# Kernel tuning notes

Hardware: AMD Instinct MI355X
Metric: run time of the kernel (lower is better)

## Reference

```python
import jax, jax.numpy as jnp
import numpy as np

NUM_EXPERTS = 8
TOP_K = 2


def setup_inputs() -> dict:
    key = jax.random.key(0)
    k0, k1, k2, k3, k4 = jax.random.split(key, 5)
    T, D, F, E = 4096, 2048, 4096, NUM_EXPERTS  # tokens, hidden, intermediate, experts
    s_in = 1.0 / np.sqrt(D).astype(np.float32)
    s_mid = 1.0 / np.sqrt(F).astype(np.float32)
    return {
        "hidden_states": jax.random.normal(k0, (T, D), jnp.float32),
        "gate_w": jax.random.normal(k1, (D, E), jnp.float32) * s_in,   # router gate (no bias)
        "w1": jax.random.normal(k2, (E, D, F), jnp.float32) * s_in,     # expert gate proj
        "w3": jax.random.normal(k3, (E, D, F), jnp.float32) * s_in,     # expert up proj
        "w2": jax.random.normal(k4, (E, F, D), jnp.float32) * s_mid,    # expert down proj
    }


def reference(hidden_states, gate_w, w1, w3, w2):
    x = hidden_states  # [T, D] (original flattens any leading dims)
    # Router: logits in fp32 (router_logits.float()), softmax over ALL experts,
    # take top-k WITHOUT renormalization (renormalize=False).
    logits = (x @ gate_w).astype(jnp.float32)            # [T, E]
    probs = jax.nn.softmax(logits, axis=-1)              # [T, E]
    topk_w, topk_i = jax.lax.top_k(probs, TOP_K)         # [T, K]
    # Dense combine weights: zero for non-selected experts. [T, E]
    combine = jnp.sum(
        jax.nn.one_hot(topk_i, NUM_EXPERTS, dtype=x.dtype) * topk_w[..., None],
        axis=1,
    )

    # SwiGLU experts, vmapped over the expert axis (fixed, small E).
    def expert_fn(w1e, w3e, w2e):
        return (jax.nn.silu(x @ w1e) * (x @ w3e)) @ w2e  # [T, D]

    expert_out = jax.vmap(expert_fn)(w1, w3, w2)         # [E, T, D]
    return jnp.einsum("te,etd->td", combine, expert_out)  # [T, D]
```

## Files before the change

kernel.cpp:

```cpp
#include <hip/hip_runtime.h>
#include <hip/hip_bf16.h>

#define TK 4096
#define DD 2048
#define FF 4096
#define NE 8
#define BM 128
#define BN 128
#define BKR 32
#define BKP 64

typedef __attribute__((ext_vector_type(8))) short bf16x8;
typedef __attribute__((ext_vector_type(4))) short bf16x4;
typedef __attribute__((ext_vector_type(4))) float f32x4;

__device__ __forceinline__ unsigned short f2bf(float f) {
  return __builtin_bit_cast(unsigned short, __float2bfloat16(f));
}
__device__ __forceinline__ float bf2f(unsigned short u) {
  return __builtin_bit_cast(float, (unsigned)u << 16);
}

__device__ __forceinline__ void gl16(const unsigned short* g, unsigned short* l) {
  __builtin_amdgcn_global_load_lds(
      (const __attribute__((address_space(1))) unsigned int*)g,
      (__attribute__((address_space(3))) unsigned int*)l, 16, 0, 0);
}

#define VMCNT(n) asm volatile("s_waitcnt vmcnt(" #n ")" ::: "memory")
#define SBAR()   __builtin_amdgcn_s_barrier()

__device__ __forceinline__ int g_swz(int row) { return ((row >> 1) & 3) ^ ((row >> 3) & 3); }
__device__ __forceinline__ int swzoff(int row, int bir) {
  return row * 64 + ((((bir >> 4) ^ g_swz(row)) & 3) << 4) + (bir & 15);
}
__device__ __forceinline__ int permB(int f) {
  return (f & 0x60) | ((f & 3) << 3) | ((f >> 2) & 7);
}

__global__ void k_router(const float* __restrict__ x, const float* __restrict__ gw,
                         int* __restrict__ cnt, int* __restrict__ ltok,
                         float* __restrict__ lw, unsigned short* __restrict__ xb,
                         int2* __restrict__ t2s) {
  int tok = (blockIdx.x * blockDim.x + threadIdx.x) >> 6;
  int lane = threadIdx.x & 63;
  if (tok >= TK) return;
  const float* xr = x + (size_t)tok * DD;
  float a0=0,a1=0,a2=0,a3=0,a4=0,a5=0,a6=0,a7=0;
  for (int p = 0; p < DD / 256; ++p) {
    int d0 = p * 256 + lane * 4;
    f32x4 xv = *(const f32x4*)(xr + d0);
    if (xb) {
      bf16x4 t;
      t[0] = (short)f2bf(xv[0]); t[1] = (short)f2bf(xv[1]);
      t[2] = (short)f2bf(xv[2]); t[3] = (short)f2bf(xv[3]);
      *(bf16x4*)(xb + (size_t)tok * DD + d0) = t;
    }
#pragma unroll
    for (int j = 0; j < 4; ++j) {
      float xs = xv[j];
      const f32x4* g = (const f32x4*)(gw + (size_t)(d0 + j) * NE);
      f32x4 g0 = g[0], g1 = g[1];
      a0 += xs * g0[0]; a1 += xs * g0[1]; a2 += xs * g0[2]; a3 += xs * g0[3];
      a4 += xs * g1[0]; a5 += xs * g1[1]; a6 += xs * g1[2]; a7 += xs * g1[3];
    }
  }
#pragma unroll
  for (int s = 32; s > 0; s >>= 1) {
    a0 += __shfl_xor(a0, s, 64); a1 += __shfl_xor(a1, s, 64);
    a2 += __shfl_xor(a2, s, 64); a3 += __shfl_xor(a3, s, 64);
    a4 += __shfl_xor(a4, s, 64); a5 += __shfl_xor(a5, s, 64);
    a6 += __shfl_xor(a6, s, 64); a7 += __shfl_xor(a7, s, 64);
  }
  if (lane == 0) {
    float p_[NE] = {a0, a1, a2, a3, a4, a5, a6, a7};
    float m = p_[0];
#pragma unroll
    for (int e = 1; e < NE; ++e) m = fmaxf(m, p_[e]);
    float ssum = 0.f;
#pragma unroll
    for (int e = 0; e < NE; ++e) { p_[e] = __expf(p_[e] - m); ssum += p_[e]; }
    float inv = 1.f / ssum;
    int i1 = 0; float b1 = p_[0];
#pragma unroll
    for (int e = 1; e < NE; ++e) if (p_[e] > b1) { b1 = p_[e]; i1 = e; }
    int i2 = -1; float b2 = -1.f;
#pragma unroll
    for (int e = 0; e < NE; ++e) if (e != i1 && p_[e] > b2) { b2 = p_[e]; i2 = e; }
    int s1 = atomicAdd(&cnt[i1], 1);
    ltok[i1 * TK + s1] = tok; lw[i1 * TK + s1] = b1 * inv;
    int s2 = atomicAdd(&cnt[i2], 1);
    ltok[i2 * TK + s2] = tok; lw[i2 * TK + s2] = b2 * inv;
    if (t2s) t2s[tok] = make_int2(i1 * TK + s1, i2 * TK + s2);
  }
}

__global__ void k_prefix(const int* __restrict__ cnt, int* __restrict__ off) {
  if (threadIdx.x == 0) {
    int a = 0;
#pragma unroll
    for (int e = 0; e < NE; ++e) { off[e] = a; a += cnt[e]; }
    off[NE] = a;
  }
}

__global__ __launch_bounds__(256)
void k_tr(const float* __restrict__ src0, unsigned short* __restrict__ dst0,
          int R, int C) {
  const int e = blockIdx.z;
  const float* src = src0 + (size_t)e * R * C;
  unsigned short* dst = dst0 + (size_t)e * R * C;
  const int tid = threadIdx.x;
  const int w = tid >> 6, lane = tid & 63;
  const int r0 = blockIdx.y * 256 + w * 64 + (lane >> 3) * 8;
  const int c0 = blockIdx.x * 32 + (lane & 7) * 4;
  f32x4 v[8];
#pragma unroll
  for (int j = 0; j < 8; ++j) v[j] = *(const f32x4*)(src + (size_t)(r0 + j) * C + c0);
#pragma unroll
  for (int jc = 0; jc < 4; ++jc) {
    bf16x8 o;
#pragma unroll
    for (int j = 0; j < 8; ++j) o[j] = (short)f2bf(v[j][jc]);
    *(bf16x8*)(dst + (size_t)(c0 + jc) * R + r0) = o;
  }
}

__global__ __launch_bounds__(256)
void k_tr13(const float* __restrict__ w1, const float* __restrict__ w3,
            unsigned short* __restrict__ d1, unsigned short* __restrict__ d3) {
  const int z = blockIdx.z;
  const int e = z & (NE - 1);
  const float* src = (z < NE ? w1 : w3) + (size_t)e * DD * FF;
  unsigned short* dst = (z < NE ? d1 : d3) + (size_t)e * DD * FF;
  const int tid = threadIdx.x;
  const int w = tid >> 6, lane = tid & 63;
  const int r0 = blockIdx.y * 256 + w * 64 + (lane >> 3) * 8;
  const int c0 = blockIdx.x * 32 + (lane & 7) * 4;
  f32x4 v[8];
#pragma unroll
  for (int j = 0; j < 8; ++j) v[j] = *(const f32x4*)(src + (size_t)(r0 + j) * FF + c0);
#pragma unroll
  for (int jc = 0; jc < 4; ++jc) {
    bf16x8 o;
#pragma unroll
    for (int j = 0; j < 8; ++j) o[j] = (short)f2bf(v[j][jc]);
    *(bf16x8*)(dst + (size_t)(c0 + jc) * DD + r0) = o;
  }
}

__global__ __launch_bounds__(256)
void k_comb(const unsigned short* __restrict__ O, const int2* __restrict__ t2s,
            const int* __restrict__ off, float* __restrict__ out) {
  const int idx = blockIdx.x * 256 + threadIdx.x;
  const int t = idx >> 8;
  const int d0 = (idx & 255) * 8;
  const int2 v = t2s[t];
  const int s1 = off[v.x >> 12] + (v.x & (TK - 1));
  const int s2 = off[v.y >> 12] + (v.y & (TK - 1));
  bf16x8 a = *(const bf16x8*)(O + (size_t)s1 * DD + d0);
  bf16x8 b = *(const bf16x8*)(O + (size_t)s2 * DD + d0);
  f32x4 r0, r1;
#pragma unroll
  for (int j = 0; j < 4; ++j) {
    r0[j] = bf2f((unsigned short)a[j]) + bf2f((unsigned short)b[j]);
    r1[j] = bf2f((unsigned short)a[j + 4]) + bf2f((unsigned short)b[j + 4]);
  }
  float* o = out + (size_t)t * DD + d0;
  *(f32x4*)o = r0;
  *(f32x4*)(o + 4) = r1;
}


__global__ __launch_bounds__(256, 2)
void k_gemm1g(const unsigned short* __restrict__ xb, const unsigned short* __restrict__ w1t,
              const unsigned short* __restrict__ w3t, const int* __restrict__ cnt,
              const int* __restrict__ off, const int* __restrict__ ltok,
              const float* __restrict__ lw, unsigned short* __restrict__ H) {
  const int e = blockIdx.z;
  const int ce = cnt[e];
  const int m0 = blockIdx.y * BM;
  if (m0 >= ce) return;
  const int n0 = blockIdx.x * BN;
  const int tid = threadIdx.x, lane = tid & 63, w = tid >> 6;
  const int wr = w >> 1, wc = w & 1;
  const unsigned short* W1 = w1t + (size_t)e * FF * DD;
  const unsigned short* W3 = w3t + (size_t)e * FF * DD;
  const int base = off[e];

  __shared__ __align__(16) unsigned short As[BM * BKP];
  __shared__ __align__(16) unsigned short B1s[2][BM * BKP];
  __shared__ __align__(16) unsigned short B3s[2][BM * BKP];

  const int swz8 = ((lane & 7) ^ ((lane >> 3) & 7)) * 8;
  const unsigned short *aSrc[4], *b1Src[4], *b3Src[4];
#pragma unroll
  for (int i = 0; i < 4; ++i) {
    int row = w * 32 + i * 8 + (lane >> 3);
    int gm = m0 + row;
    int tok = (gm < ce) ? ltok[e * TK + gm] : ltok[e * TK];
    aSrc[i]  = xb + (size_t)tok * DD + swz8;
    b1Src[i] = W1 + (size_t)(n0 + row) * DD + swz8;
    b3Src[i] = W3 + (size_t)(n0 + row) * DD + swz8;
  }

  const int kc = lane >> 4;
  int aOff[4][2], bOff[4][2];
#pragma unroll
  for (int m = 0; m < 4; ++m) {
    int row = wr * 64 + m * 16 + (lane & 15);
#pragma unroll
    for (int kk = 0; kk < 2; ++kk) {
      int c = kk * 4 + kc;
      aOff[m][kk] = row * 128 + ((c ^ (row & 7)) << 4);
    }
  }
#pragma unroll
  for (int n = 0; n < 4; ++n) {
    int row = wc * 64 + n * 16 + (lane & 15);
#pragma unroll
    for (int kk = 0; kk < 2; ++kk) {
      int c = kk * 4 + kc;
      bOff[n][kk] = row * 128 + ((c ^ (row & 7)) << 4);
    }
  }

  f32x4 acc1[4][4], acc3[4][4];
#pragma unroll
  for (int m = 0; m < 4; ++m)
#pragma unroll
    for (int n = 0; n < 4; ++n)
#pragma unroll
      for (int j = 0; j < 4; ++j) { acc1[m][n][j] = 0.f; acc3[m][n][j] = 0.f; }

  auto STAGE_A = [&]() {
#pragma unroll
    for (int i = 0; i < 4; ++i) {
      gl16(aSrc[i], &As[(w * 4 + i) * 512]);
      aSrc[i] += BKP;
    }
  };
  auto STAGE_B = [&](int buf) {
#pragma unroll
    for (int i = 0; i < 4; ++i) {
      const int seg = w * 4 + i;
      gl16(b1Src[i], &B1s[buf][seg * 512]);
      gl16(b3Src[i], &B3s[buf][seg * 512]);
      b1Src[i] += BKP; b3Src[i] += BKP;
    }
  };
  auto COMPUTE = [&](int buf) {
#pragma unroll
    for (int kk = 0; kk < 2; ++kk) {
      bf16x8 af[4];
#pragma unroll
      for (int m = 0; m < 4; ++m) af[m] = *(const bf16x8*)((const char*)As + aOff[m][kk]);
#pragma unroll
      for (int n = 0; n < 4; ++n) {
        bf16x8 b1 = *(const bf16x8*)((const char*)B1s[buf] + bOff[n][kk]);
        bf16x8 b3 = *(const bf16x8*)((const char*)B3s[buf] + bOff[n][kk]);
#pragma unroll
        for (int m = 0; m < 4; ++m) {
          acc1[m][n] = __builtin_amdgcn_mfma_f32_16x16x32_bf16(af[m], b1, acc1[m][n], 0, 0, 0);
          acc3[m][n] = __builtin_amdgcn_mfma_f32_16x16x32_bf16(af[m], b3, acc3[m][n], 0, 0, 0);
        }
      }
    }
  };

  const int NT = DD / BKP;
  STAGE_A();
  STAGE_B(0);
  int b = 0;
  for (int kt = 0; kt < NT - 1; ++kt) {
    STAGE_B(b ^ 1);
    VMCNT(8);
    SBAR();
    COMPUTE(b);
    SBAR();
    STAGE_A();
    b ^= 1;
  }
  VMCNT(0);
  SBAR();
  COMPUTE(b);

#pragma unroll
  for (int m = 0; m < 4; ++m) {
    const int rbase = wr * 64 + m * 16 + ((lane >> 4) << 2);
    float wts[4]; bool val[4];
#pragma unroll
    for (int j = 0; j < 4; ++j) {
      int r = m0 + rbase + j;
      val[j] = r < ce;
      wts[j] = val[j] ? lw[e * TK + r] : 0.f;
    }
#pragma unroll
    for (int n = 0; n < 4; ++n) {
      const int col = n0 + wc * 64 + n * 16 + (lane & 15);
#pragma unroll
      for (int j = 0; j < 4; ++j) {
        if (!val[j]) continue;
        float s1 = acc1[m][n][j], s3 = acc3[m][n][j];
        float h = s1 / (1.f + __expf(-s1)) * s3 * wts[j];
        H[(size_t)(base + m0 + rbase + j) * FF + col] = f2bf(h);
      }
    }
  }
}

__global__ __launch_bounds__(256, 3)
void k_gemm2g(const unsigned short* __restrict__ H, const unsigned short* __restrict__ w2t,
              const int* __restrict__ cnt, const int* __restrict__ off,
              unsigned short* __restrict__ O) {
  const int e = blockIdx.z;
  const int ce = cnt[e];
  const int m0 = blockIdx.y * BM;
  if (m0 >= ce) return;
  const int n0 = blockIdx.x * BN;
  const int tid = threadIdx.x, lane = tid & 63, w = tid >> 6;
  const int wr = w >> 1, wc = w & 1;
  const unsigned short* W2 = w2t + (size_t)e * DD * FF;
  const int base = off[e];

  __shared__ __align__(16) unsigned short As[BM * BKP];
  __shared__ __align__(16) unsigned short Bs[2][BN * BKP];

  const int swz8 = ((lane & 7) ^ ((lane >> 3) & 7)) * 8;
  const unsigned short *aSrc[4], *bSrc[4];
#pragma unroll
  for (int i = 0; i < 4; ++i) {
    int row = w * 32 + i * 8 + (lane >> 3);
    int gm = m0 + row;
    int hr = (gm < ce) ? gm : 0;
    aSrc[i] = H + (size_t)(base + hr) * FF + swz8;
    bSrc[i] = W2 + (size_t)(n0 + row) * FF + swz8;
  }

  const int kc = lane >> 4;
  int aOff[4][2], bOff[4][2];
#pragma unroll
  for (int m = 0; m < 4; ++m) {
    int row = wr * 64 + m * 16 + (lane & 15);
#pragma unroll
    for (int kk = 0; kk < 2; ++kk) {
      int c = kk * 4 + kc;
      aOff[m][kk] = row * 128 + ((c ^ (row & 7)) << 4);
    }
  }
#pragma unroll
  for (int n = 0; n < 4; ++n) {
    int row = wc * 64 + n * 16 + (lane & 15);
#pragma unroll
    for (int kk = 0; kk < 2; ++kk) {
      int c = kk * 4 + kc;
      bOff[n][kk] = row * 128 + ((c ^ (row & 7)) << 4);
    }
  }

  f32x4 acc[4][4];
#pragma unroll
  for (int m = 0; m < 4; ++m)
#pragma unroll
    for (int n = 0; n < 4; ++n)
#pragma unroll
      for (int j = 0; j < 4; ++j) acc[m][n][j] = 0.f;

  auto STAGE_A = [&]() {
#pragma unroll
    for (int i = 0; i < 4; ++i) {
      gl16(aSrc[i], &As[(w * 4 + i) * 512]);
      aSrc[i] += BKP;
    }
  };
  auto STAGE_B = [&](int buf) {
#pragma unroll
    for (int i = 0; i < 4; ++i) {
      gl16(bSrc[i], &Bs[buf][(w * 4 + i) * 512]);
      bSrc[i] += BKP;
    }
  };
  auto COMPUTE = [&](int buf) {
#pragma unroll
    for (int kk = 0; kk < 2; ++kk) {
      bf16x8 af[4];
#pragma unroll
      for (int m = 0; m < 4; ++m) af[m] = *(const bf16x8*)((const char*)As + aOff[m][kk]);
#pragma unroll
      for (int n = 0; n < 4; ++n) {
        bf16x8 bf = *(const bf16x8*)((const char*)Bs[buf] + bOff[n][kk]);
#pragma unroll
        for (int m = 0; m < 4; ++m)
          acc[m][n] = __builtin_amdgcn_mfma_f32_16x16x32_bf16(af[m], bf, acc[m][n], 0, 0, 0);
      }
    }
  };

  const int NT = FF / BKP;
  STAGE_A();
  STAGE_B(0);
  int b = 0;
  for (int kt = 0; kt < NT - 1; ++kt) {
    STAGE_B(b ^ 1);
    VMCNT(4);
    SBAR();
    COMPUTE(b);
    SBAR();
    STAGE_A();
    b ^= 1;
  }
  VMCNT(0);
  SBAR();
  COMPUTE(b);

#pragma unroll
  for (int m = 0; m < 4; ++m) {
    const int rbase = wr * 64 + m * 16 + ((lane >> 4) << 2);
#pragma unroll
    for (int n = 0; n < 4; ++n) {
      const int col = n0 + wc * 64 + n * 16 + (lane & 15);
#pragma unroll
      for (int j = 0; j < 4; ++j) {
        int r = m0 + rbase + j;
        if (r < ce) O[(size_t)(base + r) * DD + col] = f2bf(acc[m][n][j]);
      }
    }
  }
}

__global__ __launch_bounds__(256, 2)
void k_gemm1(const float* __restrict__ x, const float* __restrict__ w1g,
             const float* __restrict__ w3g, const int* __restrict__ cnt,
             const int* __restrict__ off, const int* __restrict__ ltok,
             const float* __restrict__ lw, unsigned short* __restrict__ H) {
  const int e = blockIdx.z;
  const int ce = cnt[e];
  const int m0 = blockIdx.y * BM;
  if (m0 >= ce) return;
  const int n0 = blockIdx.x * BN;
  const int tid = threadIdx.x, lane = tid & 63, wv = tid >> 6;
  const int wr = wv >> 1, wc = wv & 1;
  const float* W1 = w1g + (size_t)e * DD * FF;
  const float* W3 = w3g + (size_t)e * DD * FF;
  const int base = off[e];

  __shared__ unsigned short As[2][BM * BKR];
  __shared__ unsigned short B1s[2][BN * BKR];
  __shared__ unsigned short B3s[2][BN * BKR];

  const int arow = tid >> 1, ah = tid & 1;
  const float* xrow = (m0 + arow < ce) ? (x + (size_t)ltok[e * TK + (m0 + arow)] * DD) : nullptr;
  const int dblk = tid >> 5, fblk = tid & 31;

  const int kb = (lane >> 4) * 16;
  int aOff[4], bOff[4], wAoff[4], wBoff[4];
#pragma unroll
  for (int m = 0; m < 4; ++m) aOff[m] = swzoff(wr * 64 + m * 16 + (lane & 15), kb);
#pragma unroll
  for (int n = 0; n < 4; ++n) bOff[n] = swzoff(permB(wc * 64 + n * 16 + (lane & 15)), kb);
#pragma unroll
  for (int j = 0; j < 4; ++j) {
    wAoff[j] = swzoff(arow, ah * 32 + j * 8);
    wBoff[j] = swzoff(permB(fblk * 4 + j), dblk * 8);
  }

  f32x4 acc1[4][4], acc3[4][4];
#pragma unroll
  for (int m = 0; m < 4; ++m)
#pragma unroll
    for (int n = 0; n < 4; ++n)
#pragma unroll
      for (int j = 0; j < 4; ++j) { acc1[m][n][j] = 0.f; acc3[m][n][j] = 0.f; }

  f32x4 av[4], v1[4], v3[4];

  auto LOAD = [&](int kt) {
    const int k0 = kt * BKR;
#pragma unroll
    for (int j = 0; j < 4; ++j) {
      if (xrow) av[j] = *(const f32x4*)(xrow + k0 + ah * 16 + j * 4);
      else { av[j][0] = 0.f; av[j][1] = 0.f; av[j][2] = 0.f; av[j][3] = 0.f; }
    }
    const float* p1 = W1 + (size_t)(k0 + dblk * 4) * FF + (n0 + fblk * 4);
    const float* p3 = W3 + (size_t)(k0 + dblk * 4) * FF + (n0 + fblk * 4);
#pragma unroll
    for (int r = 0; r < 4; ++r) {
      v1[r] = *(const f32x4*)(p1 + (size_t)r * FF);
      v3[r] = *(const f32x4*)(p3 + (size_t)r * FF);
    }
  };
  auto STORE = [&](int buf) {
#pragma unroll
    for (int j = 0; j < 4; ++j) {
      bf16x4 t;
      t[0] = (short)f2bf(av[j][0]); t[1] = (short)f2bf(av[j][1]);
      t[2] = (short)f2bf(av[j][2]); t[3] = (short)f2bf(av[j][3]);
      *(bf16x4*)((char*)As[buf] + wAoff[j]) = t;
    }
#pragma unroll
    for (int j = 0; j < 4; ++j) {
      bf16x4 t1, t3;
      t1[0] = (short)f2bf(v1[0][j]); t1[1] = (short)f2bf(v1[1][j]);
      t1[2] = (short)f2bf(v1[2][j]); t1[3] = (short)f2bf(v1[3][j]);
      t3[0] = (short)f2bf(v3[0][j]); t3[1] = (short)f2bf(v3[1][j]);
      t3[2] = (short)f2bf(v3[2][j]); t3[3] = (short)f2bf(v3[3][j]);
      *(bf16x4*)((char*)B1s[buf] + wBoff[j]) = t1;
      *(bf16x4*)((char*)B3s[buf] + wBoff[j]) = t3;
    }
  };

  LOAD(0); STORE(0);
  int cur = 0;
  const int NT = DD / BKR;
  for (int kt = 0; kt < NT; ++kt) {
    if (kt + 1 < NT) LOAD(kt + 1);
    __syncthreads();
    bf16x8 af[4];
#pragma unroll
    for (int m = 0; m < 4; ++m) af[m] = *(const bf16x8*)((const char*)As[cur] + aOff[m]);
#pragma unroll
    for (int n = 0; n < 4; ++n) {
      bf16x8 b1 = *(const bf16x8*)((const char*)B1s[cur] + bOff[n]);
      bf16x8 b3 = *(const bf16x8*)((const char*)B3s[cur] + bOff[n]);
#pragma unroll
      for (int m = 0; m < 4; ++m) {
        acc1[m][n] = __builtin_amdgcn_mfma_f32_16x16x32_bf16(af[m], b1, acc1[m][n], 0, 0, 0);
        acc3[m][n] = __builtin_amdgcn_mfma_f32_16x16x32_bf16(af[m], b3, acc3[m][n], 0, 0, 0);
      }
    }
    if (kt + 1 < NT) STORE(cur ^ 1);
    cur ^= 1;
  }

#pragma unroll
  for (int m = 0; m < 4; ++m) {
    const int rbase = wr * 64 + m * 16 + ((lane >> 4) << 2);
    float wts[4]; bool val[4];
#pragma unroll
    for (int j = 0; j < 4; ++j) {
      int r = m0 + rbase + j;
      val[j] = r < ce;
      wts[j] = val[j] ? lw[e * TK + r] : 0.f;
    }
#pragma unroll
    for (int n = 0; n < 4; ++n) {
      const int col = n0 + wc * 64 + n * 16 + (lane & 15);
#pragma unroll
      for (int j = 0; j < 4; ++j) {
        if (!val[j]) continue;
        float s1 = acc1[m][n][j], s3 = acc3[m][n][j];
        float h = s1 / (1.f + __expf(-s1)) * s3 * wts[j];
        H[(size_t)(base + m0 + rbase + j) * FF + col] = f2bf(h);
      }
    }
  }
}

__global__ __launch_bounds__(256, 2)
void k_gemm2(const unsigned short* __restrict__ H, const float* __restrict__ w2g,
             const int* __restrict__ cnt, const int* __restrict__ off,
             const int* __restrict__ ltok, float* __restrict__ out) {
  const int e = blockIdx.z;
  const int ce = cnt[e];
  const int m0 = blockIdx.y * BM;
  if (m0 >= ce) return;
  const int n0 = blockIdx.x * BN;
  const int tid = threadIdx.x, lane = tid & 63, wv = tid >> 6;
  const int wr = wv >> 1, wc = wv & 1;
  const float* W2 = w2g + (size_t)e * FF * DD;
  const int base = off[e];

  __shared__ unsigned short As[2][BM * BKR];
  __shared__ unsigned short Bs[2][BN * BKR];

  const int arow = tid >> 1, ah = tid & 1;
  const bool aval = (m0 + arow) < ce;
  const unsigned short* hrow = H + (size_t)(base + m0 + arow) * FF;
  const int kblk = tid >> 5, nblk = tid & 31;

  const int kb = (lane >> 4) * 16;
  int aOff[4], bOff[4], wAoff[2], wBoff[4];
#pragma unroll
  for (int m = 0; m < 4; ++m) aOff[m] = swzoff(wr * 64 + m * 16 + (lane & 15), kb);
#pragma unroll
  for (int n = 0; n < 4; ++n) bOff[n] = swzoff(permB(wc * 64 + n * 16 + (lane & 15)), kb);
#pragma unroll
  for (int j = 0; j < 2; ++j) wAoff[j] = swzoff(arow, ah * 32 + j * 16);
#pragma unroll
  for (int j = 0; j < 4; ++j) wBoff[j] = swzoff(permB(nblk * 4 + j), kblk * 8);

  f32x4 acc[4][4];
#pragma unroll
  for (int m = 0; m < 4; ++m)
#pragma unroll
    for (int n = 0; n < 4; ++n)
#pragma unroll
      for (int j = 0; j < 4; ++j) acc[m][n][j] = 0.f;

  bf16x8 av2[2];
  f32x4 wv2[4];

  auto LOAD = [&](int kt) {
    const int k0 = kt * BKR;
#pragma unroll
    for (int j = 0; j < 2; ++j) {
      if (aval) av2[j] = *(const bf16x8*)(hrow + k0 + ah * 16 + j * 8);
      else {
#pragma unroll
        for (int q = 0; q < 8; ++q) av2[j][q] = 0;
      }
    }
    const float* p = W2 + (size_t)(k0 + kblk * 4) * DD + (n0 + nblk * 4);
#pragma unroll
    for (int r = 0; r < 4; ++r) wv2[r] = *(const f32x4*)(p + (size_t)r * DD);
  };
  auto STORE = [&](int buf) {
#pragma unroll
    for (int j = 0; j < 2; ++j) *(bf16x8*)((char*)As[buf] + wAoff[j]) = av2[j];
#pragma unroll
    for (int j = 0; j < 4; ++j) {
      bf16x4 t;
      t[0] = (short)f2bf(wv2[0][j]); t[1] = (short)f2bf(wv2[1][j]);
      t[2] = (short)f2bf(wv2[2][j]); t[3] = (short)f2bf(wv2[3][j]);
      *(bf16x4*)((char*)Bs[buf] + wBoff[j]) = t;
    }
  };

  LOAD(0); STORE(0);
  int cur = 0;
  const int NT = FF / BKR;
  for (int kt = 0; kt < NT; ++kt) {
    if (kt + 1 < NT) LOAD(kt + 1);
    __syncthreads();
    bf16x8 af[4];
#pragma unroll
    for (int m = 0; m < 4; ++m) af[m] = *(const bf16x8*)((const char*)As[cur] + aOff[m]);
#pragma unroll
    for (int n = 0; n < 4; ++n) {
      bf16x8 bf = *(const bf16x8*)((const char*)Bs[cur] + bOff[n]);
#pragma unroll
      for (int m = 0; m < 4; ++m)
        acc[m][n] = __builtin_amdgcn_mfma_f32_16x16x32_bf16(af[m], bf, acc[m][n], 0, 0, 0);
    }
    if (kt + 1 < NT) STORE(cur ^ 1);
    cur ^= 1;
  }

#pragma unroll
  for (int m = 0; m < 4; ++m) {
    const int rbase = wr * 64 + m * 16 + ((lane >> 4) << 2);
    int toks[4]; bool val[4];
#pragma unroll
    for (int j = 0; j < 4; ++j) {
      int r = m0 + rbase + j;
      val[j] = r < ce;
      toks[j] = val[j] ? ltok[e * TK + r] : 0;
    }
#pragma unroll
    for (int n = 0; n < 4; ++n) {
      const int col = n0 + wc * 64 + n * 16 + (lane & 15);
#pragma unroll
      for (int j = 0; j < 4; ++j)
        if (val[j]) atomicAdd(out + (size_t)toks[j] * DD + col, acc[m][n][j]);
    }
  }
}

extern "C" void kernel_launch(void* const* d_in, const int* in_sizes, int n_in,
                              void* d_out, int out_size, void* d_ws, size_t ws_size,
                              hipStream_t stream) {
  const float* x  = (const float*)d_in[0];
  const float* gw = (const float*)d_in[1];
  const float* w1 = (const float*)d_in[2];
  const float* w3 = (const float*)d_in[3];
  const float* w2 = (const float*)d_in[4];
  float* out = (float*)d_out;

  char* ws = (char*)d_ws;
  int*   cnt  = (int*)(ws);
  int*   off  = (int*)(ws + 64);
  int*   ltok = (int*)(ws + 256);
  float* lw   = (float*)(ws + 256 + (size_t)NE * TK * 4);
  int2*  t2s  = (int2*)(ws + 512 * 1024);

  const size_t SZ_XB = (size_t)TK * DD * 2;
  const size_t SZ_W  = (size_t)NE * DD * FF * 2;
  const size_t SZ_H  = (size_t)2 * TK * FF * 2;
  size_t o = (size_t)1 << 20;
  unsigned short* xb  = (unsigned short*)(ws + o); o += SZ_XB;
  unsigned short* w1t = (unsigned short*)(ws + o); o += SZ_W;
  unsigned short* w3t = (unsigned short*)(ws + o); o += SZ_W;
  unsigned short* w2t = (unsigned short*)(ws + o); o += SZ_W;
  unsigned short* Hg  = (unsigned short*)(ws + o); o += SZ_H;
  unsigned short* O   = w1t;
  const bool full = (ws_size >= o);

  hipMemsetAsync(cnt, 0, 64, stream);

  if (full) {
    k_router<<<dim3(TK / 4), 256, 0, stream>>>(x, gw, cnt, ltok, lw, xb, t2s);
    k_prefix<<<dim3(1), 64, 0, stream>>>(cnt, off);
    k_tr13<<<dim3(FF / 32, DD / 256, 2 * NE), 256, 0, stream>>>(w1, w3, w1t, w3t);
    k_tr<<<dim3(DD / 32, FF / 256, NE), 256, 0, stream>>>(w2, w2t, FF, DD);
    k_gemm1g<<<dim3(FF / BN, TK / BM, NE), 256, 0, stream>>>(xb, w1t, w3t, cnt, off, ltok, lw, Hg);
    k_gemm2g<<<dim3(DD / BN, TK / BM, NE), 256, 0, stream>>>(Hg, w2t, cnt, off, O);
    k_comb<<<dim3(TK * DD / 8 / 256), 256, 0, stream>>>(O, t2s, off, out);
  } else {
    unsigned short* H = (unsigned short*)(ws + ((size_t)1 << 20));
    if (ws_size < ((size_t)1 << 20) + SZ_H) return;
    hipMemsetAsync(d_out, 0, (size_t)out_size * 4, stream);
    k_router<<<dim3(TK / 4), 256, 0, stream>>>(x, gw, cnt, ltok, lw,
                                               (unsigned short*)nullptr, (int2*)nullptr);
    k_prefix<<<dim3(1), 64, 0, stream>>>(cnt, off);
    k_gemm1<<<dim3(FF / BN, TK / BM, NE), 256, 0, stream>>>(x, w1, w3, cnt, off, ltok, lw, H);
    k_gemm2<<<dim3(DD / BN, TK / BM, NE), 256, 0, stream>>>(H, w2, cnt, off, ltok, out);
  }
}
```

Measured before the change: 920.9 us.

## Load gathered token rows directly into registers, bypassing LDS in gate/up GEMM

```diff
diff --git a/kernel.cpp b/kernel.cpp
--- a/kernel.cpp
+++ b/kernel.cpp
@@ -171,7 +171,6 @@
   *(f32x4*)(o + 4) = r1;
 }
 
-
 __global__ __launch_bounds__(256, 2)
 void k_gemm1g(const unsigned short* __restrict__ xb, const unsigned short* __restrict__ w1t,
               const unsigned short* __restrict__ w3t, const int* __restrict__ cnt,
@@ -185,36 +184,31 @@
   const int tid = threadIdx.x, lane = tid & 63, w = tid >> 6;
   const int wr = w >> 1, wc = w & 1;
   const unsigned short* W1 = w1t + (size_t)e * FF * DD;
-  const unsigned short* W3 = w3t + (size_t)e * FF * DD;
+  const size_t W3OFF = (size_t)NE * FF * DD;
   const int base = off[e];
 
-  __shared__ __align__(16) unsigned short As[BM * BKP];
   __shared__ __align__(16) unsigned short B1s[2][BM * BKP];
   __shared__ __align__(16) unsigned short B3s[2][BM * BKP];
 
   const int swz8 = ((lane & 7) ^ ((lane >> 3) & 7)) * 8;
-  const unsigned short *aSrc[4], *b1Src[4], *b3Src[4];
+  const unsigned short* b1Src[4];
 #pragma unroll
   for (int i = 0; i < 4; ++i) {
     int row = w * 32 + i * 8 + (lane >> 3);
+    b1Src[i] = W1 + (size_t)(n0 + row) * DD + swz8;
+  }
+
+  const unsigned short* xrowp[4];
+#pragma unroll
+  for (int m = 0; m < 4; ++m) {
+    int row = wr * 64 + m * 16 + (lane & 15);
     int gm = m0 + row;
     int tok = (gm < ce) ? ltok[e * TK + gm] : ltok[e * TK];
-    aSrc[i]  = xb + (size_t)tok * DD + swz8;
-    b1Src[i] = W1 + (size_t)(n0 + row) * DD + swz8;
-    b3Src[i] = W3 + (size_t)(n0 + row) * DD + swz8;
+    xrowp[m] = xb + (size_t)tok * DD + (lane >> 4) * 8;
   }
 
   const int kc = lane >> 4;
-  int aOff[4][2], bOff[4][2];
-#pragma unroll
-  for (int m = 0; m < 4; ++m) {
-    int row = wr * 64 + m * 16 + (lane & 15);
-#pragma unroll
-    for (int kk = 0; kk < 2; ++kk) {
-      int c = kk * 4 + kc;
-      aOff[m][kk] = row * 128 + ((c ^ (row & 7)) << 4);
-    }
-  }
+  int bOff[4][2];
 #pragma unroll
   for (int n = 0; n < 4; ++n) {
     int row = wc * 64 + n * 16 + (lane & 15);
@@ -233,57 +227,57 @@
 #pragma unroll
       for (int j = 0; j < 4; ++j) { acc1[m][n][j] = 0.f; acc3[m][n][j] = 0.f; }
 
-  auto STAGE_A = [&]() {
-#pragma unroll
-    for (int i = 0; i < 4; ++i) {
-      gl16(aSrc[i], &As[(w * 4 + i) * 512]);
-      aSrc[i] += BKP;
-    }
-  };
+  bf16x8 afA[4][2], afB[4][2];
+
   auto STAGE_B = [&](int buf) {
 #pragma unroll
     for (int i = 0; i < 4; ++i) {
       const int seg = w * 4 + i;
-      gl16(b1Src[i], &B1s[buf][seg * 512]);
-      gl16(b3Src[i], &B3s[buf][seg * 512]);
-      b1Src[i] += BKP; b3Src[i] += BKP;
-    }
-  };
-  auto COMPUTE = [&](int buf) {
+      gl16(b1Src[i],         &B1s[buf][seg * 512]);
+      gl16(b1Src[i] + W3OFF, &B3s[buf][seg * 512]);
+      b1Src[i] += BKP;
+    }
+  };
+  auto LOADA = [&](bf16x8 (&af)[4][2], int kt) {
+#pragma unroll
+    for (int m = 0; m < 4; ++m)
+#pragma unroll
+      for (int kk = 0; kk < 2; ++kk)
+        af[m][kk] = *(const bf16x8*)(xrowp[m] + kt * BKP + kk * 32);
+  };
+  auto COMPUTE = [&](int buf, bf16x8 (&af)[4][2]) {
 #pragma unroll
     for (int kk = 0; kk < 2; ++kk) {
-      bf16x8 af[4];
-#pragma unroll
-      for (int m = 0; m < 4; ++m) af[m] = *(const bf16x8*)((const char*)As + aOff[m][kk]);
 #pragma unroll
       for (int n = 0; n < 4; ++n) {
         bf16x8 b1 = *(const bf16x8*)((const char*)B1s[buf] + bOff[n][kk]);
         bf16x8 b3 = *(const bf16x8*)((const char*)B3s[buf] + bOff[n][kk]);
 #pragma unroll
         for (int m = 0; m < 4; ++m) {
-          acc1[m][n] = __builtin_amdgcn_mfma_f32_16x16x32_bf16(af[m], b1, acc1[m][n], 0, 0, 0);
-          acc3[m][n] = __builtin_amdgcn_mfma_f32_16x16x32_bf16(af[m], b3, acc3[m][n], 0, 0, 0);
+          acc1[m][n] = __builtin_amdgcn_mfma_f32_16x16x32_bf16(af[m][kk], b1, acc1[m][n], 0, 0, 0);
+          acc3[m][n] = __builtin_amdgcn_mfma_f32_16x16x32_bf16(af[m][kk], b3, acc3[m][n], 0, 0, 0);
         }
       }
     }
   };
 
   const int NT = DD / BKP;
-  STAGE_A();
   STAGE_B(0);
-  int b = 0;
-  for (int kt = 0; kt < NT - 1; ++kt) {
-    STAGE_B(b ^ 1);
-    VMCNT(8);
+  LOADA(afA, 0);
+  for (int kt = 0; kt < NT; kt += 2) {
+    STAGE_B(1);
+    LOADA(afB, kt + 1);
+    VMCNT(16);
     SBAR();
-    COMPUTE(b);
+    COMPUTE(0, afA);
     SBAR();
-    STAGE_A();
-    b ^= 1;
-  }
-  VMCNT(0);
-  SBAR();
-  COMPUTE(b);
+    STAGE_B(0);
+    LOADA(afA, kt + 2);
+    VMCNT(16);
+    SBAR();
+    COMPUTE(1, afB);
+    SBAR();
+  }
 
 #pragma unroll
   for (int m = 0; m < 4; ++m) {
```

New measurement: 1.245 ms. 1.35x slower.

## Prefetch A fragments to registers so next A tile loads overlap MFMAs

Applied to the files above, without the earlier changes.

```diff
diff --git a/kernel.cpp b/kernel.cpp
--- a/kernel.cpp
+++ b/kernel.cpp
@@ -28,6 +28,7 @@
 }
 
 #define VMCNT(n) asm volatile("s_waitcnt vmcnt(" #n ")" ::: "memory")
+#define LGKM0()  asm volatile("s_waitcnt lgkmcnt(0)" ::: "memory")
 #define SBAR()   __builtin_amdgcn_s_barrier()
 
 __device__ __forceinline__ int g_swz(int row) { return ((row >> 1) & 3) ^ ((row >> 3) & 3); }
@@ -249,41 +250,45 @@
       b1Src[i] += BKP; b3Src[i] += BKP;
     }
   };
-  auto COMPUTE = [&](int buf) {
+
+  const int NT = DD / BKP;
+  STAGE_B(0);
+  STAGE_A();
+  int b = 0;
+  for (int kt = 0; kt < NT; ++kt) {
+    const bool more = (kt + 1 < NT);
+    if (more) {
+      STAGE_B(b ^ 1);
+      VMCNT(8);
+    } else {
+      VMCNT(0);
+    }
+    SBAR();
+    bf16x8 af[4][2];
+#pragma unroll
+    for (int kk = 0; kk < 2; ++kk)
+#pragma unroll
+      for (int m = 0; m < 4; ++m)
+        af[m][kk] = *(const bf16x8*)((const char*)As + aOff[m][kk]);
+    LGKM0();
+    SBAR();
+    if (more) STAGE_A();
 #pragma unroll
     for (int kk = 0; kk < 2; ++kk) {
-      bf16x8 af[4];
-#pragma unroll
-      for (int m = 0; m < 4; ++m) af[m] = *(const bf16x8*)((const char*)As + aOff[m][kk]);
 #pragma unroll
       for (int n = 0; n < 4; ++n) {
-        bf16x8 b1 = *(const bf16x8*)((const char*)B1s[buf] + bOff[n][kk]);
-        bf16x8 b3 = *(const bf16x8*)((const char*)B3s[buf] + bOff[n][kk]);
+        bf16x8 b1 = *(const bf16x8*)((const char*)B1s[b] + bOff[n][kk]);
+        bf16x8 b3 = *(const bf16x8*)((const char*)B3s[b] + bOff[n][kk]);
 #pragma unroll
         for (int m = 0; m < 4; ++m) {
-          acc1[m][n] = __builtin_amdgcn_mfma_f32_16x16x32_bf16(af[m], b1, acc1[m][n], 0, 0, 0);
-          acc3[m][n] = __builtin_amdgcn_mfma_f32_16x16x32_bf16(af[m], b3, acc3[m][n], 0, 0, 0);
+          acc1[m][n] = __builtin_amdgcn_mfma_f32_16x16x32_bf16(af[m][kk], b1, acc1[m][n], 0, 0, 0);
+          acc3[m][n] = __builtin_amdgcn_mfma_f32_16x16x32_bf16(af[m][kk], b3, acc3[m][n], 0, 0, 0);
         }
       }
     }
-  };
-
-  const int NT = DD / BKP;
-  STAGE_A();
-  STAGE_B(0);
-  int b = 0;
-  for (int kt = 0; kt < NT - 1; ++kt) {
-    STAGE_B(b ^ 1);
-    VMCNT(8);
     SBAR();
-    COMPUTE(b);
-    SBAR();
-    STAGE_A();
     b ^= 1;
   }
-  VMCNT(0);
-  SBAR();
-  COMPUTE(b);
 
 #pragma unroll
   for (int m = 0; m < 4; ++m) {
@@ -380,38 +385,42 @@
       bSrc[i] += BKP;
     }
   };
-  auto COMPUTE = [&](int buf) {
+
+  const int NT = FF / BKP;
+  STAGE_B(0);
+  STAGE_A();
+  int b = 0;
+  for (int kt = 0; kt < NT; ++kt) {
+    const bool more = (kt + 1 < NT);
+    if (more) {
+      STAGE_B(b ^ 1);
+      VMCNT(4);
+    } else {
+      VMCNT(0);
+    }
+    SBAR();
+    bf16x8 af[4][2];
+#pragma unroll
+    for (int kk = 0; kk < 2; ++kk)
+#pragma unroll
+      for (int m = 0; m < 4; ++m)
+        af[m][kk] = *(const bf16x8*)((const char*)As + aOff[m][kk]);
+    LGKM0();
+    SBAR();
+    if (more) STAGE_A();
 #pragma unroll
     for (int kk = 0; kk < 2; ++kk) {
-      bf16x8 af[4];
-#pragma unroll
-      for (int m = 0; m < 4; ++m) af[m] = *(const bf16x8*)((const char*)As + aOff[m][kk]);
 #pragma unroll
       for (int n = 0; n < 4; ++n) {
-        bf16x8 bf = *(const bf16x8*)((const char*)Bs[buf] + bOff[n][kk]);
+        bf16x8 bf = *(const bf16x8*)((const char*)Bs[b] + bOff[n][kk]);
 #pragma unroll
         for (int m = 0; m < 4; ++m)
-          acc[m][n] = __builtin_amdgcn_mfma_f32_16x16x32_bf16(af[m], bf, acc[m][n], 0, 0, 0);
+          acc[m][n] = __builtin_amdgcn_mfma_f32_16x16x32_bf16(af[m][kk], bf, acc[m][n], 0, 0, 0);
       }
     }
-  };
-
-  const int NT = FF / BKP;
-  STAGE_A();
-  STAGE_B(0);
-  int b = 0;
-  for (int kt = 0; kt < NT - 1; ++kt) {
-    STAGE_B(b ^ 1);
-    VMCNT(4);
     SBAR();
-    COMPUTE(b);
-    SBAR();
-    STAGE_A();
     b ^= 1;
   }
-  VMCNT(0);
-  SBAR();
-  COMPUTE(b);
 
 #pragma unroll
   for (int m = 0; m < 4; ++m) {
```

Result: no change. 933.5 us (+1.4%).
